# Optimization experiments

Measured on AMD Instinct MI355X. Metric: run time of the kernel, lower is better.

## Reference

```python
import jax, jax.numpy as jnp
import numpy as np

N_NODES = 100000
N_EDGES = 1600000
IN_F = 32
HID = 128


def setup_inputs() -> dict:
    key = jax.random.key(0)
    ks = jax.random.split(key, 8)
    x = jax.random.normal(ks[0], (N_NODES, IN_F), dtype=jnp.float32)
    edge_index = jax.random.randint(ks[1], (2, N_EDGES), 0, N_NODES, dtype=jnp.int64)
    # Glorot-ish scaled weights
    W1 = jax.random.normal(ks[2], (IN_F, HID), dtype=jnp.float32) / np.sqrt(IN_F)
    b1 = jnp.zeros((HID,), dtype=jnp.float32)
    W2 = jax.random.normal(ks[3], (HID, HID), dtype=jnp.float32) / np.sqrt(HID)
    b2 = jnp.zeros((HID,), dtype=jnp.float32)
    W3 = jax.random.normal(ks[4], (HID, IN_F), dtype=jnp.float32) / np.sqrt(HID)
    b3 = jnp.zeros((IN_F,), dtype=jnp.float32)
    return {"x": x, "edge_index": edge_index, "W1": W1, "b1": b1,
            "W2": W2, "b2": b2, "W3": W3, "b3": b3}


def _gcn_norm(edge_index, n_nodes):
    # Add self-loops (PyG GCNConv default) and compute symmetric normalization
    loops = jnp.arange(n_nodes, dtype=edge_index.dtype)
    src = jnp.concatenate([edge_index[0], loops])
    dst = jnp.concatenate([edge_index[1], loops])
    ones = jnp.ones(src.shape[0], dtype=jnp.float32)
    deg = jax.ops.segment_sum(ones, dst, num_segments=n_nodes)
    deg_inv_sqrt = jnp.where(deg > 0, jax.lax.rsqrt(deg), 0.0)
    norm = deg_inv_sqrt[src] * deg_inv_sqrt[dst]  # [E + N]
    return src, dst, norm


def _gcn_conv(x, src, dst, norm, W, b, n_nodes):
    h = x @ W                                # [N, out] transform first (smaller msgs when out<in)
    msg = h[src] * norm[:, None]             # gather + edge-wise scale  [E+N, out]
    out = jax.ops.segment_sum(msg, dst, num_segments=n_nodes)  # scatter-add
    return out + b


def reference(x, edge_index, W1, b1, W2, b2, W3, b3):
    n = x.shape[0]
    src, dst, norm = _gcn_norm(edge_index, n)
    h = jax.nn.relu(_gcn_conv(x, src, dst, norm, W1, b1, n))
    h = jax.nn.relu(_gcn_conv(h, src, dst, norm, W2, b2, n))
    h = jax.nn.relu(_gcn_conv(h, src, dst, norm, W3, b3, n))
    return h
```

## Files before the change

kernel.cpp:

```cpp
#include <hip/hip_runtime.h>
#include <hip/hip_fp16.h>

#define N_NODES 100000
#define N_EDGES 1600000
#define IN_F 32
#define HID 128
#define BSHIFT 9
#define BSIZE 512
#define NBUCK 196
#define EPB 8192
#define NBB 196

typedef _Float16 half8 __attribute__((ext_vector_type(8)));
typedef float floatx4 __attribute__((ext_vector_type(4)));

static __device__ __forceinline__ void pack2(_Float16* dst, float a, float b) {
    union { _Float16 h[2]; unsigned u; } p;
    p.h[0] = (_Float16)a; p.h[1] = (_Float16)b;
    *(unsigned*)dst = p.u;
}


__global__ __launch_bounds__(256) void k_bcount(const int* __restrict__ dst,
                                                int* __restrict__ bcnt) {
    __shared__ int hist[256];
    hist[threadIdx.x] = 0;
    __syncthreads();
    const int e0 = blockIdx.x * EPB;
#pragma unroll 4
    for (int k = 0; k < 32; ++k) {
        int e = e0 + k * 256 + threadIdx.x;
        if (e < N_EDGES) atomicAdd(&hist[dst[e] >> BSHIFT], 1);
    }
    __syncthreads();
    int c = hist[threadIdx.x];
    if (c > 0) atomicAdd(&bcnt[threadIdx.x], c);
}

__global__ __launch_bounds__(256) void k_bscan(const int* __restrict__ bcnt,
                                               int* __restrict__ bbase,
                                               int* __restrict__ bcur) {
    __shared__ int s[256];
    int v = (threadIdx.x < NBUCK) ? bcnt[threadIdx.x] : 0;
    s[threadIdx.x] = v;
    __syncthreads();
    for (int off = 1; off < 256; off <<= 1) {
        int t = (threadIdx.x >= off) ? s[threadIdx.x - off] : 0;
        __syncthreads();
        s[threadIdx.x] += t;
        __syncthreads();
    }
    if (threadIdx.x < NBUCK) {
        int ex = s[threadIdx.x] - v;
        bbase[threadIdx.x] = ex;
        bcur[threadIdx.x]  = ex;
    }
    if (threadIdx.x == 0) bbase[NBUCK] = N_EDGES;
}

__global__ __launch_bounds__(256) void k_bucket(const int* __restrict__ src,
                                                const int* __restrict__ dst,
                                                int* __restrict__ bcur,
                                                unsigned* __restrict__ rec) {
    __shared__ int hist[256];
    __shared__ int lbase[256];
    const int e0 = blockIdx.x * EPB;
    hist[threadIdx.x] = 0;
    __syncthreads();

    unsigned rk[32]; short bk[32];
#pragma unroll
    for (int k = 0; k < 32; ++k) {
        int e = e0 + k * 256 + threadIdx.x;
        if (e < N_EDGES) {
            int d = dst[e];
            int b = d >> BSHIFT;
            bk[k] = (short)b;
            rk[k] = ((unsigned)src[e] << BSHIFT) | (unsigned)(d & (BSIZE - 1));
            atomicAdd(&hist[b], 1);
        } else bk[k] = -1;
    }
    __syncthreads();
    int c = hist[threadIdx.x];
    lbase[threadIdx.x] = (c > 0) ? atomicAdd(&bcur[threadIdx.x], c) : 0;
    __syncthreads();
    hist[threadIdx.x] = 0;
    __syncthreads();
#pragma unroll
    for (int k = 0; k < 32; ++k) {
        if (bk[k] >= 0) {
            int off = atomicAdd(&hist[bk[k]], 1);
            rec[lbase[bk[k]] + off] = rk[k];
        }
    }
}

__global__ __launch_bounds__(256) void k_fill3(const unsigned* __restrict__ rec,
                                               const int* __restrict__ bbase,
                                               int* __restrict__ ideg,
                                               int* __restrict__ cursor,
                                               int* __restrict__ col) {
    __shared__ int lcnt[BSIZE];
    __shared__ int lcur[BSIZE];
    __shared__ int s[256];
    const int b = blockIdx.x;
    const int n0 = b << BSHIFT;
    const int rbeg = bbase[b];
    const int rend = bbase[b + 1];

    lcnt[threadIdx.x] = 0;
    lcnt[threadIdx.x + 256] = 0;
    __syncthreads();
    for (int i = rbeg + threadIdx.x; i < rend; i += 256)
        atomicAdd(&lcnt[rec[i] & (BSIZE - 1)], 1);
    __syncthreads();

    int a0 = lcnt[2 * threadIdx.x], a1 = lcnt[2 * threadIdx.x + 1];
    int pv = a0 + a1;
    s[threadIdx.x] = pv;
    __syncthreads();
    for (int off = 1; off < 256; off <<= 1) {
        int t = (threadIdx.x >= off) ? s[threadIdx.x - off] : 0;
        __syncthreads();
        s[threadIdx.x] += t;
        __syncthreads();
    }
    int ex = s[threadIdx.x] - pv;
    lcur[2 * threadIdx.x]     = rbeg + ex;
    lcur[2 * threadIdx.x + 1] = rbeg + ex + a0;
    __syncthreads();

    for (int t = threadIdx.x; t < BSIZE; t += 256) {
        int n = n0 + t;
        if (n < N_NODES) {
            ideg[n]   = lcnt[t];
            cursor[n] = lcur[t];
        }
    }
    __syncthreads();
    for (int i = rbeg + threadIdx.x; i < rend; i += 256) {
        unsigned r = rec[i];
        int slot = atomicAdd(&lcur[r & (BSIZE - 1)], 1);
        col[slot] = (int)(r >> BSHIFT);
    }
}


__global__ void k_prescale(const float2* __restrict__ x, const int* __restrict__ ideg,
                           __half2* __restrict__ T) {
    int tid = blockIdx.x * 256 + threadIdx.x;
    if (tid >= N_NODES * 16) return;
    int i = tid >> 4;
    float dis = rsqrtf(1.0f + (float)ideg[i]);
    float2 v = x[tid];
    T[tid] = __floats2half2_rn(v.x * dis, v.y * dis);
}


__global__ __launch_bounds__(256) void k_gather32_pre(
    const int* __restrict__ cursor, const int* __restrict__ ideg,
    const int* __restrict__ col, const _Float16* __restrict__ T,
    _Float16* __restrict__ OUT) {
    const int lane = threadIdx.x & 63;
    const int slot = lane >> 2;
    const int fl   = lane & 3;
    const int wid  = blockIdx.x * 4 + (threadIdx.x >> 6);
    const int wstride = gridDim.x * 4;

    for (int node = wid; node < N_NODES; node += wstride) {
        int begin = cursor[node];
        int d     = ideg[node];
        int end   = begin + d;
        float acc[8];
        if (slot == 0) {
            half8 v = *(const half8*)(T + (size_t)node * IN_F + fl * 8);
#pragma unroll
            for (int i = 0; i < 8; ++i) acc[i] = (float)v[i];
        } else {
#pragma unroll
            for (int i = 0; i < 8; ++i) acc[i] = 0.f;
        }
        for (int e = begin; e < end; e += 16) {
            int ee = e + slot;
            if (ee < end) {
                int s = col[ee];
                half8 v = *(const half8*)(T + (size_t)s * IN_F + fl * 8);
#pragma unroll
                for (int i = 0; i < 8; ++i) acc[i] += (float)v[i];
            }
        }
#pragma unroll
        for (int m = 4; m < 64; m <<= 1)
#pragma unroll
            for (int i = 0; i < 8; ++i) acc[i] += __shfl_xor(acc[i], m, 64);
        if (slot == 0) {
            float dis = rsqrtf(1.0f + (float)d);
            half8 o;
#pragma unroll
            for (int i = 0; i < 8; ++i) o[i] = (_Float16)(acc[i] * dis);
            *(half8*)(OUT + (size_t)node * IN_F + fl * 8) = o;
        }
    }
}

__global__ __launch_bounds__(256) void k_gather32_fin(
    const int* __restrict__ cursor, const int* __restrict__ ideg,
    const int* __restrict__ col, const _Float16* __restrict__ T,
    const float* __restrict__ b, float* __restrict__ OUT) {
    const int lane = threadIdx.x & 63;
    const int slot = lane >> 2;
    const int fl   = lane & 3;
    const int wid  = blockIdx.x * 4 + (threadIdx.x >> 6);
    const int wstride = gridDim.x * 4;

    float4 bb0 = *(const float4*)(b + fl * 8);
    float4 bb1 = *(const float4*)(b + fl * 8 + 4);
    float bias[8] = {bb0.x, bb0.y, bb0.z, bb0.w, bb1.x, bb1.y, bb1.z, bb1.w};

    for (int node = wid; node < N_NODES; node += wstride) {
        int begin = cursor[node];
        int d     = ideg[node];
        int end   = begin + d;
        float acc[8];
        if (slot == 0) {
            half8 v = *(const half8*)(T + (size_t)node * IN_F + fl * 8);
#pragma unroll
            for (int i = 0; i < 8; ++i) acc[i] = (float)v[i];
        } else {
#pragma unroll
            for (int i = 0; i < 8; ++i) acc[i] = 0.f;
        }
        for (int e = begin; e < end; e += 16) {
            int ee = e + slot;
            if (ee < end) {
                int s = col[ee];
                half8 v = *(const half8*)(T + (size_t)s * IN_F + fl * 8);
#pragma unroll
                for (int i = 0; i < 8; ++i) acc[i] += (float)v[i];
            }
        }
#pragma unroll
        for (int m = 4; m < 64; m <<= 1)
#pragma unroll
            for (int i = 0; i < 8; ++i) acc[i] += __shfl_xor(acc[i], m, 64);
        if (slot == 0) {
            float dis = rsqrtf(1.0f + (float)d);
            float o[8];
#pragma unroll
            for (int i = 0; i < 8; ++i) {
                float v = acc[i] * dis + bias[i];
                o[i] = v > 0.f ? v : 0.f;
            }
            float* op = OUT + (size_t)node * IN_F + fl * 8;
            *(float4*)op       = make_float4(o[0], o[1], o[2], o[3]);
            *(float4*)(op + 4) = make_float4(o[4], o[5], o[6], o[7]);
        }
    }
}

__global__ __launch_bounds__(256) void k_gather128(
    const int* __restrict__ cursor, const int* __restrict__ ideg,
    const int* __restrict__ col, const _Float16* __restrict__ T,
    const float* __restrict__ b, _Float16* __restrict__ OUT) {
    const int lane = threadIdx.x & 63;
    const int slot = lane >> 4;
    const int fl   = lane & 15;
    const int wid  = blockIdx.x * 4 + (threadIdx.x >> 6);
    const int wstride = gridDim.x * 4;

    float4 bb0 = *(const float4*)(b + fl * 8);
    float4 bb1 = *(const float4*)(b + fl * 8 + 4);
    float bias[8] = {bb0.x, bb0.y, bb0.z, bb0.w, bb1.x, bb1.y, bb1.z, bb1.w};

    for (int node = wid; node < N_NODES; node += wstride) {
        int begin = cursor[node];
        int d     = ideg[node];
        int end   = begin + d;
        float acc[8];
        if (slot == 0) {
            half8 v = *(const half8*)(T + (size_t)node * HID + fl * 8);
#pragma unroll
            for (int i = 0; i < 8; ++i) acc[i] = (float)v[i];
        } else {
#pragma unroll
            for (int i = 0; i < 8; ++i) acc[i] = 0.f;
        }
        for (int e = begin; e < end; e += 8) {
            int ee0 = e + slot;
            int ee1 = e + 4 + slot;
            if (ee1 < end) {
                int s0 = col[ee0];
                int s1 = col[ee1];
                half8 v0 = *(const half8*)(T + (size_t)s0 * HID + fl * 8);
                half8 v1 = *(const half8*)(T + (size_t)s1 * HID + fl * 8);
#pragma unroll
                for (int i = 0; i < 8; ++i) acc[i] += (float)v0[i] + (float)v1[i];
            } else if (ee0 < end) {
                int s0 = col[ee0];
                half8 v0 = *(const half8*)(T + (size_t)s0 * HID + fl * 8);
#pragma unroll
                for (int i = 0; i < 8; ++i) acc[i] += (float)v0[i];
            }
        }
#pragma unroll
        for (int m = 16; m < 64; m <<= 1)
#pragma unroll
            for (int i = 0; i < 8; ++i) acc[i] += __shfl_xor(acc[i], m, 64);
        if (slot == 0) {
            float dis = rsqrtf(1.0f + (float)d);
            half8 o;
#pragma unroll
            for (int i = 0; i < 8; ++i) {
                float v = acc[i] * dis + bias[i];
                o[i] = (_Float16)(v > 0.f ? v : 0.f);
            }
            *(half8*)(OUT + (size_t)node * HID + fl * 8) = o;
        }
    }
}


__global__ __launch_bounds__(256) void k_xform1_mfma(
    const _Float16* __restrict__ z, const float* __restrict__ W,
    const float* __restrict__ bias, _Float16* __restrict__ Hh) {
    __shared__ _Float16 Wt[128 * 40];
    for (int idx = threadIdx.x; idx < 2048; idx += 256) {
        int n = idx & 127, k = (idx >> 7) * 2;
        pack2(&Wt[n * 40 + k], W[k * HID + n], W[(k + 1) * HID + n]);
    }
    __syncthreads();

    const int lane = threadIdx.x & 63;
    const int wave = threadIdx.x >> 6;
    const int m16 = lane & 15, quad = lane >> 4;
    const int row0 = blockIdx.x * 64 + wave * 16;
    if (row0 >= N_NODES) return;

    int arow = row0 + m16; if (arow >= N_NODES) arow = N_NODES - 1;
    half8 a = *(const half8*)(z + (size_t)arow * IN_F + quad * 8);

    floatx4 acc[8];
#pragma unroll
    for (int t = 0; t < 8; ++t) acc[t] = (floatx4){0.f, 0.f, 0.f, 0.f};
#pragma unroll
    for (int t = 0; t < 8; ++t) {
        half8 b = *(const half8*)&Wt[(t * 16 + m16) * 40 + quad * 8];
        acc[t] = __builtin_amdgcn_mfma_f32_16x16x32_f16(a, b, acc[t], 0, 0, 0);
    }
#pragma unroll
    for (int t = 0; t < 8; ++t) {
        int c = t * 16 + m16;
        float bj = bias[c];
#pragma unroll
        for (int r = 0; r < 4; ++r) {
            int row = row0 + quad * 4 + r;
            if (row < N_NODES) {
                float v = acc[t][r] + bj;
                Hh[(size_t)row * HID + c] = (_Float16)(v > 0.f ? v : 0.f);
            }
        }
    }
}

__global__ __launch_bounds__(256) void k_xform2_mfma(
    const _Float16* __restrict__ H, const float* __restrict__ W,
    const int* __restrict__ ideg, _Float16* __restrict__ T) {
    __shared__ _Float16 Wt[128 * 136];
    for (int idx = threadIdx.x; idx < 8192; idx += 256) {
        int n = idx & 127, k = (idx >> 7) * 2;
        pack2(&Wt[n * 136 + k], W[k * HID + n], W[(k + 1) * HID + n]);
    }
    __syncthreads();

    const int lane = threadIdx.x & 63;
    const int wave = threadIdx.x >> 6;
    const int m16 = lane & 15, quad = lane >> 4;
    const int row0 = blockIdx.x * 64 + wave * 16;
    if (row0 >= N_NODES) return;

    int arow = row0 + m16; if (arow >= N_NODES) arow = N_NODES - 1;
    const _Float16* hp = H + (size_t)arow * HID + quad * 8;
    half8 a[4];
#pragma unroll
    for (int kk = 0; kk < 4; ++kk) a[kk] = *(const half8*)(hp + kk * 32);

    floatx4 acc[8];
#pragma unroll
    for (int t = 0; t < 8; ++t) acc[t] = (floatx4){0.f, 0.f, 0.f, 0.f};
#pragma unroll
    for (int t = 0; t < 8; ++t) {
        const _Float16* wp = &Wt[(t * 16 + m16) * 136 + quad * 8];
#pragma unroll
        for (int kk = 0; kk < 4; ++kk) {
            half8 b = *(const half8*)(wp + kk * 32);
            acc[t] = __builtin_amdgcn_mfma_f32_16x16x32_f16(a[kk], b, acc[t], 0, 0, 0);
        }
    }
    float dis[4];
#pragma unroll
    for (int r = 0; r < 4; ++r) {
        int row = row0 + quad * 4 + r;
        dis[r] = (row < N_NODES) ? rsqrtf(1.0f + (float)ideg[row]) : 0.f;
    }
#pragma unroll
    for (int t = 0; t < 8; ++t) {
        int c = t * 16 + m16;
#pragma unroll
        for (int r = 0; r < 4; ++r) {
            int row = row0 + quad * 4 + r;
            if (row < N_NODES)
                T[(size_t)row * HID + c] = (_Float16)(acc[t][r] * dis[r]);
        }
    }
}

__global__ __launch_bounds__(256) void k_xform3_mfma(
    const _Float16* __restrict__ H, const float* __restrict__ W,
    const int* __restrict__ ideg, _Float16* __restrict__ T) {
    __shared__ _Float16 Wt[32 * 136];
    for (int idx = threadIdx.x; idx < 2048; idx += 256) {
        int n = idx & 31, k = (idx >> 5) * 2;
        pack2(&Wt[n * 136 + k], W[k * IN_F + n], W[(k + 1) * IN_F + n]);
    }
    __syncthreads();

    const int lane = threadIdx.x & 63;
    const int wave = threadIdx.x >> 6;
    const int m16 = lane & 15, quad = lane >> 4;
    const int row0 = blockIdx.x * 64 + wave * 16;
    if (row0 >= N_NODES) return;

    int arow = row0 + m16; if (arow >= N_NODES) arow = N_NODES - 1;
    const _Float16* hp = H + (size_t)arow * HID + quad * 8;
    half8 a[4];
#pragma unroll
    for (int kk = 0; kk < 4; ++kk) a[kk] = *(const half8*)(hp + kk * 32);

    floatx4 acc[2];
#pragma unroll
    for (int t = 0; t < 2; ++t) acc[t] = (floatx4){0.f, 0.f, 0.f, 0.f};
#pragma unroll
    for (int t = 0; t < 2; ++t) {
        const _Float16* wp = &Wt[(t * 16 + m16) * 136 + quad * 8];
#pragma unroll
        for (int kk = 0; kk < 4; ++kk) {
            half8 b = *(const half8*)(wp + kk * 32);
            acc[t] = __builtin_amdgcn_mfma_f32_16x16x32_f16(a[kk], b, acc[t], 0, 0, 0);
        }
    }
    float dis[4];
#pragma unroll
    for (int r = 0; r < 4; ++r) {
        int row = row0 + quad * 4 + r;
        dis[r] = (row < N_NODES) ? rsqrtf(1.0f + (float)ideg[row]) : 0.f;
    }
#pragma unroll
    for (int t = 0; t < 2; ++t) {
        int c = t * 16 + m16;
#pragma unroll
        for (int r = 0; r < 4; ++r) {
            int row = row0 + quad * 4 + r;
            if (row < N_NODES)
                T[(size_t)row * IN_F + c] = (_Float16)(acc[t][r] * dis[r]);
        }
    }
}


extern "C" void kernel_launch(void* const* d_in, const int* in_sizes, int n_in,
                              void* d_out, int out_size, void* d_ws, size_t ws_size,
                              hipStream_t stream) {
    const float* x  = (const float*)d_in[0];
    const int*   ei = (const int*)d_in[1];
    const float* W1 = (const float*)d_in[2];
    const float* b1 = (const float*)d_in[3];
    const float* W2 = (const float*)d_in[4];
    const float* b2 = (const float*)d_in[5];
    const float* W3 = (const float*)d_in[6];
    const float* b3 = (const float*)d_in[7];
    float* out = (float*)d_out;

    const int* src = ei;
    const int* dst = ei + N_EDGES;

    int*      ideg   = (int*)d_ws;
    int*      cursor = ideg + 102400;
    int*      bcnt   = cursor + 102400;
    int*      bbase  = bcnt + 256;
    int*      bcur   = bbase + 256;
    int*      col    = bcur + 256;
    unsigned* rec    = (unsigned*)(col + N_EDGES);
    _Float16* t1h    = (_Float16*)(rec + N_EDGES);
    _Float16* z      = t1h + (size_t)N_NODES * IN_F;
    _Float16* H1h    = z + (size_t)N_NODES * IN_F;
    _Float16* T2h    = H1h + (size_t)N_NODES * HID;
    _Float16* H2h    = T2h + (size_t)N_NODES * HID;

    const int xgrid = (N_NODES + 63) / 64;

    hipMemsetAsync(bcnt, 0, 256 * sizeof(int), stream);
    k_bcount<<<NBB, 256, 0, stream>>>(dst, bcnt);
    k_bscan<<<1, 256, 0, stream>>>(bcnt, bbase, bcur);
    k_bucket<<<NBB, 256, 0, stream>>>(src, dst, bcur, rec);
    k_fill3<<<NBUCK, 256, 0, stream>>>(rec, bbase, ideg, cursor, col);

    k_prescale<<<(N_NODES * 16 + 255) / 256, 256, 0, stream>>>(
        (const float2*)x, ideg, (__half2*)t1h);
    k_gather32_pre<<<2048, 256, 0, stream>>>(cursor, ideg, col, t1h, z);
    k_xform1_mfma<<<xgrid, 256, 0, stream>>>(z, W1, b1, H1h);

    k_xform2_mfma<<<xgrid, 256, 0, stream>>>(H1h, W2, ideg, T2h);
    k_gather128<<<2048, 256, 0, stream>>>(cursor, ideg, col, T2h, b2, H2h);

    k_xform3_mfma<<<xgrid, 256, 0, stream>>>(H2h, W3, ideg, T2h);
    k_gather32_fin<<<2048, 256, 0, stream>>>(cursor, ideg, col, T2h, b3, out);
}
```

Baseline: 333.9 us.

## Pad CSR rows to multiples of 16 with a zero dummy node

The CSR build now pads each node's neighbour list to a multiple of 16 entries. Padding slots point to a dummy node index N_NODES, whose feature row is zeroed in each producer kernel. With that guarantee, the gather kernels drop their per-edge bounds checks and run full 16-wide batches; the 128-wide gather reads four column indices at once with an int4 load. The cost is a larger column array and extra gathers of the zero row for padded slots. The workspace is also re-laid out so the rec buffer aliases the first feature buffer.

```diff
diff --git a/kernel.cpp b/kernel.cpp
--- a/kernel.cpp
+++ b/kernel.cpp
@@ -10,6 +10,7 @@
 #define NBUCK 196
 #define EPB 8192
 #define NBB 196
+#define COLSZ 3206144
 
 typedef _Float16 half8 __attribute__((ext_vector_type(8)));
 typedef float floatx4 __attribute__((ext_vector_type(4)));
@@ -102,11 +103,13 @@
                                                int* __restrict__ col) {
     __shared__ int lcnt[BSIZE];
     __shared__ int lcur[BSIZE];
+    __shared__ int lend[BSIZE];
     __shared__ int s[256];
     const int b = blockIdx.x;
     const int n0 = b << BSHIFT;
     const int rbeg = bbase[b];
     const int rend = bbase[b + 1];
+    const int pbeg = ((rbeg + 15) & ~15) + (16 * BSIZE) * b;
 
     lcnt[threadIdx.x] = 0;
     lcnt[threadIdx.x + 256] = 0;
@@ -116,7 +119,8 @@
     __syncthreads();
 
     int a0 = lcnt[2 * threadIdx.x], a1 = lcnt[2 * threadIdx.x + 1];
-    int pv = a0 + a1;
+    int p0 = (a0 + 15) & ~15, p1 = (a1 + 15) & ~15;
+    int pv = p0 + p1;
     s[threadIdx.x] = pv;
     __syncthreads();
     for (int off = 1; off < 256; off <<= 1) {
@@ -126,8 +130,10 @@
         __syncthreads();
     }
     int ex = s[threadIdx.x] - pv;
-    lcur[2 * threadIdx.x]     = rbeg + ex;
-    lcur[2 * threadIdx.x + 1] = rbeg + ex + a0;
+    int c0 = pbeg + ex;
+    int c1 = c0 + p0;
+    lcur[2 * threadIdx.x]     = c0;  lend[2 * threadIdx.x]     = c0 + p0;
+    lcur[2 * threadIdx.x + 1] = c1;  lend[2 * threadIdx.x + 1] = c1 + p1;
     __syncthreads();
 
     for (int t = threadIdx.x; t < BSIZE; t += 256) {
@@ -143,11 +149,18 @@
         int slot = atomicAdd(&lcur[r & (BSIZE - 1)], 1);
         col[slot] = (int)(r >> BSHIFT);
     }
+    __syncthreads();
+    for (int t = threadIdx.x; t < BSIZE; t += 256) {
+        int e2 = lend[t];
+        for (int k = lcur[t]; k < e2; ++k) col[k] = N_NODES;
+    }
 }
 
 
 __global__ void k_prescale(const float2* __restrict__ x, const int* __restrict__ ideg,
                            __half2* __restrict__ T) {
+    if (blockIdx.x == 0 && threadIdx.x < 16)
+        ((unsigned*)(T + (size_t)N_NODES * 16))[threadIdx.x] = 0u;
     int tid = blockIdx.x * 256 + threadIdx.x;
     if (tid >= N_NODES * 16) return;
     int i = tid >> 4;
@@ -170,7 +183,7 @@
     for (int node = wid; node < N_NODES; node += wstride) {
         int begin = cursor[node];
         int d     = ideg[node];
-        int end   = begin + d;
+        int nb    = (d + 15) >> 4;
         float acc[8];
         if (slot == 0) {
             half8 v = *(const half8*)(T + (size_t)node * IN_F + fl * 8);
@@ -180,14 +193,21 @@
 #pragma unroll
             for (int i = 0; i < 8; ++i) acc[i] = 0.f;
         }
-        for (int e = begin; e < end; e += 16) {
-            int ee = e + slot;
-            if (ee < end) {
-                int s = col[ee];
-                half8 v = *(const half8*)(T + (size_t)s * IN_F + fl * 8);
-#pragma unroll
-                for (int i = 0; i < 8; ++i) acc[i] += (float)v[i];
-            }
+        const int* cp = col + begin + slot;
+        int itb = 0;
+        for (; itb + 2 <= nb; itb += 2, cp += 32) {
+            int s0 = cp[0];
+            int s1 = cp[16];
+            half8 v0 = *(const half8*)(T + (size_t)s0 * IN_F + fl * 8);
+            half8 v1 = *(const half8*)(T + (size_t)s1 * IN_F + fl * 8);
+#pragma unroll
+            for (int i = 0; i < 8; ++i) acc[i] += (float)v0[i] + (float)v1[i];
+        }
+        if (itb < nb) {
+            int s0 = cp[0];
+            half8 v0 = *(const half8*)(T + (size_t)s0 * IN_F + fl * 8);
+#pragma unroll
+            for (int i = 0; i < 8; ++i) acc[i] += (float)v0[i];
         }
 #pragma unroll
         for (int m = 4; m < 64; m <<= 1)
@@ -220,7 +240,7 @@
     for (int node = wid; node < N_NODES; node += wstride) {
         int begin = cursor[node];
         int d     = ideg[node];
-        int end   = begin + d;
+        int nb    = (d + 15) >> 4;
         float acc[8];
         if (slot == 0) {
             half8 v = *(const half8*)(T + (size_t)node * IN_F + fl * 8);
@@ -230,14 +250,21 @@
 #pragma unroll
             for (int i = 0; i < 8; ++i) acc[i] = 0.f;
         }
-        for (int e = begin; e < end; e += 16) {
-            int ee = e + slot;
-            if (ee < end) {
-                int s = col[ee];
-                half8 v = *(const half8*)(T + (size_t)s * IN_F + fl * 8);
-#pragma unroll
-                for (int i = 0; i < 8; ++i) acc[i] += (float)v[i];
-            }
+        const int* cp = col + begin + slot;
+        int itb = 0;
+        for (; itb + 2 <= nb; itb += 2, cp += 32) {
+            int s0 = cp[0];
+            int s1 = cp[16];
+            half8 v0 = *(const half8*)(T + (size_t)s0 * IN_F + fl * 8);
+            half8 v1 = *(const half8*)(T + (size_t)s1 * IN_F + fl * 8);
+#pragma unroll
+            for (int i = 0; i < 8; ++i) acc[i] += (float)v0[i] + (float)v1[i];
+        }
+        if (itb < nb) {
+            int s0 = cp[0];
+            half8 v0 = *(const half8*)(T + (size_t)s0 * IN_F + fl * 8);
+#pragma unroll
+            for (int i = 0; i < 8; ++i) acc[i] += (float)v0[i];
         }
 #pragma unroll
         for (int m = 4; m < 64; m <<= 1)
@@ -275,7 +302,7 @@
     for (int node = wid; node < N_NODES; node += wstride) {
         int begin = cursor[node];
         int d     = ideg[node];
-        int end   = begin + d;
+        int nb    = (d + 15) >> 4;
         float acc[8];
         if (slot == 0) {
             half8 v = *(const half8*)(T + (size_t)node * HID + fl * 8);
@@ -285,22 +312,16 @@
 #pragma unroll
             for (int i = 0; i < 8; ++i) acc[i] = 0.f;
         }
-        for (int e = begin; e < end; e += 8) {
-            int ee0 = e + slot;
-            int ee1 = e + 4 + slot;
-            if (ee1 < end) {
-                int s0 = col[ee0];
-                int s1 = col[ee1];
-                half8 v0 = *(const half8*)(T + (size_t)s0 * HID + fl * 8);
-                half8 v1 = *(const half8*)(T + (size_t)s1 * HID + fl * 8);
-#pragma unroll
-                for (int i = 0; i < 8; ++i) acc[i] += (float)v0[i] + (float)v1[i];
-            } else if (ee0 < end) {
-                int s0 = col[ee0];
-                half8 v0 = *(const half8*)(T + (size_t)s0 * HID + fl * 8);
-#pragma unroll
-                for (int i = 0; i < 8; ++i) acc[i] += (float)v0[i];
-            }
+        const int* cp = col + begin + slot * 4;
+        for (int itb = 0; itb < nb; ++itb, cp += 16) {
+            int4 cc = *(const int4*)cp;
+            half8 v0 = *(const half8*)(T + (size_t)cc.x * HID + fl * 8);
+            half8 v1 = *(const half8*)(T + (size_t)cc.y * HID + fl * 8);
+            half8 v2 = *(const half8*)(T + (size_t)cc.z * HID + fl * 8);
+            half8 v3 = *(const half8*)(T + (size_t)cc.w * HID + fl * 8);
+#pragma unroll
+            for (int i = 0; i < 8; ++i)
+                acc[i] += ((float)v0[i] + (float)v1[i]) + ((float)v2[i] + (float)v3[i]);
         }
 #pragma unroll
         for (int m = 16; m < 64; m <<= 1)
@@ -365,6 +386,8 @@
 __global__ __launch_bounds__(256) void k_xform2_mfma(
     const _Float16* __restrict__ H, const float* __restrict__ W,
     const int* __restrict__ ideg, _Float16* __restrict__ T) {
+    if (blockIdx.x == 0 && threadIdx.x < 64)
+        ((unsigned*)(T + (size_t)N_NODES * HID))[threadIdx.x] = 0u;
     __shared__ _Float16 Wt[128 * 136];
     for (int idx = threadIdx.x; idx < 8192; idx += 256) {
         int n = idx & 127, k = (idx >> 7) * 2;
@@ -417,6 +440,8 @@
 __global__ __launch_bounds__(256) void k_xform3_mfma(
     const _Float16* __restrict__ H, const float* __restrict__ W,
     const int* __restrict__ ideg, _Float16* __restrict__ T) {
+    if (blockIdx.x == 0 && threadIdx.x < 16)
+        ((unsigned*)(T + (size_t)N_NODES * IN_F))[threadIdx.x] = 0u;
     __shared__ _Float16 Wt[32 * 136];
     for (int idx = threadIdx.x; idx < 2048; idx += 256) {
         int n = idx & 31, k = (idx >> 5) * 2;
@@ -489,12 +514,12 @@
     int*      bbase  = bcnt + 256;
     int*      bcur   = bbase + 256;
     int*      col    = bcur + 256;
-    unsigned* rec    = (unsigned*)(col + N_EDGES);
-    _Float16* t1h    = (_Float16*)(rec + N_EDGES);
-    _Float16* z      = t1h + (size_t)N_NODES * IN_F;
+    unsigned* rec    = (unsigned*)(col + COLSZ);
+    _Float16* t1h    = (_Float16*)rec;
+    _Float16* z      = t1h + (size_t)N_NODES * IN_F + 64;
     _Float16* H1h    = z + (size_t)N_NODES * IN_F;
     _Float16* T2h    = H1h + (size_t)N_NODES * HID;
-    _Float16* H2h    = T2h + (size_t)N_NODES * HID;
+    _Float16* H2h    = T2h + (size_t)N_NODES * HID + 128;
 
     const int xgrid = (N_NODES + 63) / 64;
 
```

Result: no change. 335.1 us (+0.4%).
